# Kernel optimization log

Hardware: AMD Instinct MI355X
Metric: run time of the kernel (lower is better)

## Reference

```python
import jax, jax.numpy as jnp
import numpy as np

NX, N_IN, N_H1, N_H2, N_O = 65536, 2, 1024, 512, 1


def _deriv_tanh(h):
    # DerivTanh: 4 / (exp(-h^T) + exp(h^T))^2 == sech^2(h)^T, shape [features, nx]
    return 4.0 / (jnp.exp(-h.T) + jnp.exp(h.T)) ** 2


def setup_inputs() -> dict:
    key = jax.random.key(0)
    ks = jax.random.split(key, 7)

    def lin_init(k, fan_in, shape):
        bound = 1.0 / np.sqrt(fan_in)
        return jax.random.uniform(k, shape, jnp.float32, -bound, bound)

    x = jax.random.normal(ks[0], (NX, N_IN), jnp.float32)
    W1 = lin_init(ks[1], N_IN, (N_H1, N_IN))
    b1 = lin_init(ks[2], N_IN, (N_H1,))
    W2 = lin_init(ks[3], N_H1, (N_H2, N_H1))
    b2 = lin_init(ks[4], N_H1, (N_H2,))
    W3 = lin_init(ks[5], N_H2, (N_O, N_H2))
    b3 = lin_init(ks[6], N_H2, (N_O,))
    return {"x": x, "W1": W1, "b1": b1, "W2": W2, "b2": b2, "W3": W3, "b3": b3}


def reference(x, W1, b1, W2, b2, W3, b3):
    # Forward MLP
    h1 = x @ W1.T + b1          # [nx, h1]
    z1 = jnp.tanh(h1)
    h2 = z1 @ W2.T + b2         # [nx, h2]
    z2 = jnp.tanh(h2)
    y = z2 @ W3.T + b3          # [nx, 1]

    # Manual forward-mode derivative chain (transposed layout [features, nx])
    dz1dh1 = _deriv_tanh(h1)    # [h1, nx]
    dz2dh2 = _deriv_tanh(h2)    # [h2, nx]
    dh1dx1 = W1[:, 0][:, None]  # [h1, 1], broadcasts over nx (repeat in original)
    dh1dx2 = W1[:, 1][:, None]  # [h1, 1]

    dydx1 = (W3 @ (dz2dh2 * (W2 @ (dz1dh1 * dh1dx1)))).T  # [nx, 1]
    dydx2 = (W3 @ (dz2dh2 * (W2 @ (dz1dh1 * dh1dx2)))).T  # [nx, 1]

    v1 = dydx2
    v2 = -dydx1
    return (y, v1, v2)
```

## Files before the change

kernel.cpp:

```cpp
#include <hip/hip_runtime.h>


#define NXS    65536
#define SB     32
#define NBLK   2048
#define KSTEPS 8

typedef __attribute__((ext_vector_type(8)))  short bh8_t;
typedef __attribute__((ext_vector_type(4)))  unsigned int u32x4;
typedef __attribute__((ext_vector_type(16))) float fx16_t;
typedef unsigned int u32;

static __device__ __forceinline__ unsigned short f2bf(float f) {
  u32 u = __builtin_bit_cast(u32, f);
  u += 0x7FFFu + ((u >> 16) & 1u);
  return (unsigned short)(u >> 16);
}

static __device__ __forceinline__ u32 pkbf(float lo, float hi) {
  u32 r;
  asm("v_cvt_pk_bf16_f32 %0, %1, %2" : "=v"(r) : "v"(lo), "v"(hi));
  return r;
}

static __device__ __forceinline__ float fast_tanh(float h) {
  float e = __expf(2.0f * h);
  return 1.0f - 2.0f / (e + 1.0f);
}

__global__ void prep_all(const float* __restrict__ W2, const float* __restrict__ W1,
                         const float* __restrict__ b1, bh8_t* __restrict__ W2pT,
                         float4* __restrict__ W1b) {
  int f = blockIdx.x * 256 + threadIdx.x;
  int col = f & 31;
  int q   = (f >> 5) & 1;
  int nbk = (f >> 6) & 15;
  int kb  = f >> 10;
  const float* row = W2 + (nbk * 32 + col) * 1024 + kb * 16 + 4 * q;
  float4 lo = *(const float4*)(row);
  float4 hi = *(const float4*)(row + 8);
  bh8_t o;
  o[0] = (short)f2bf(lo.x); o[1] = (short)f2bf(lo.y);
  o[2] = (short)f2bf(lo.z); o[3] = (short)f2bf(lo.w);
  o[4] = (short)f2bf(hi.x); o[5] = (short)f2bf(hi.y);
  o[6] = (short)f2bf(hi.z); o[7] = (short)f2bf(hi.w);
  W2pT[f] = o;
  if (f < 1024) {
    float2 w = *(const float2*)(W1 + 2 * f);
    W1b[f] = make_float4(w.x, w.y, b1[f], 0.0f);
  }
}

__global__ __launch_bounds__(256, 2) void fused_kernel(
    const float* __restrict__ x,  const float4* __restrict__ W1b,
    const float* __restrict__ b2, const float* __restrict__ W3,
    const float* __restrict__ b3, const bh8_t* __restrict__ Bg,
    float* __restrict__ out)
{
  __shared__ __attribute__((aligned(16))) char smem[49152 + 1536];
  const int tid  = threadIdx.x;
  const int lane = tid & 63;
  const int wave = tid >> 6;
  const int q    = lane >> 5;
  const int col  = lane & 31;
  const int s0   = blockIdx.x * SB;

  const int gs  = tid & 31;
  const int gkb = tid >> 5;
  const float2 xv = *(const float2*)(x + 2 * (s0 + gs));
  const float x0 = xv.x, x1 = xv.y;
  const int wbase = (gs * 256) | (((gkb << 1) ^ (gs & 7)) << 4);

  fx16_t acc[3][4];
#pragma unroll
  for (int b = 0; b < 3; ++b)
#pragma unroll
    for (int nb = 0; nb < 4; ++nb)
#pragma unroll
      for (int r = 0; r < 16; ++r) acc[b][nb][r] = 0.0f;

  auto stageA = [&](int kt, char* Ab) {
    const int k16 = kt * 128 + gkb * 16;
#pragma unroll
    for (int gqp = 0; gqp < 2; ++gqp) {
      const int kL = k16 + 4 * gqp;
      u32x4 wz, wa0, wa1;
#pragma unroll
      for (int jp = 0; jp < 2; ++jp) {
        float4 cA = W1b[kL + 2 * jp];
        float4 cB = W1b[kL + 2 * jp + 1];
        float4 cC = W1b[kL + 8 + 2 * jp];
        float4 cD = W1b[kL + 8 + 2 * jp + 1];
        float hA = fmaf(x0, cA.x, fmaf(x1, cA.y, cA.z));
        float hB = fmaf(x0, cB.x, fmaf(x1, cB.y, cB.z));
        float hC = fmaf(x0, cC.x, fmaf(x1, cC.y, cC.z));
        float hD = fmaf(x0, cD.x, fmaf(x1, cD.y, cD.z));
        float zA = fast_tanh(hA), zB = fast_tanh(hB);
        float zC = fast_tanh(hC), zD = fast_tanh(hD);
        float dA = 1.f - zA * zA, dB = 1.f - zB * zB;
        float dC = 1.f - zC * zC, dD = 1.f - zD * zD;
        wz[jp]      = pkbf(zA, zB);
        wz[2 + jp]  = pkbf(zC, zD);
        wa0[jp]     = pkbf(dA * cA.x, dB * cB.x);
        wa0[2 + jp] = pkbf(dC * cC.x, dD * cD.x);
        wa1[jp]     = pkbf(dA * cA.y, dB * cB.y);
        wa1[2 + jp] = pkbf(dC * cC.y, dD * cD.y);
      }
      char* dst = Ab + (wbase ^ (gqp << 4));
      *(u32x4*)(dst)         = wz;
      *(u32x4*)(dst + 8192)  = wa0;
      *(u32x4*)(dst + 16384) = wa1;
    }
  };

  stageA(0, smem);
  __syncthreads();

  for (int kt = 0; kt < KSTEPS; ++kt) {
    char* Acur = smem + (kt & 1) * 24576;
    char* Anxt = smem + ((kt + 1) & 1) * 24576;
    if (kt + 1 < KSTEPS) stageA(kt + 1, Anxt);
    const int abase = col * 256;
#pragma unroll
    for (int ks = 0; ks < 8; ++ks) {
      const int uoff = (((2 * ks + q) ^ (col & 7)) << 4);
      bh8_t a0 = *(const bh8_t*)(Acur + abase + uoff);
      bh8_t a1 = *(const bh8_t*)(Acur + abase + 8192 + uoff);
      bh8_t a2 = *(const bh8_t*)(Acur + abase + 16384 + uoff);
      const int fb = ((kt * 8 + ks) * 16 + wave * 4) * 64 + lane;
      bh8_t bf0 = Bg[fb];
      bh8_t bf1 = Bg[fb + 64];
      bh8_t bf2 = Bg[fb + 128];
      bh8_t bf3 = Bg[fb + 192];
      __builtin_amdgcn_s_setprio(1);
      acc[0][0] = __builtin_amdgcn_mfma_f32_32x32x16_bf16(a0, bf0, acc[0][0], 0, 0, 0);
      acc[1][0] = __builtin_amdgcn_mfma_f32_32x32x16_bf16(a1, bf0, acc[1][0], 0, 0, 0);
      acc[2][0] = __builtin_amdgcn_mfma_f32_32x32x16_bf16(a2, bf0, acc[2][0], 0, 0, 0);
      acc[0][1] = __builtin_amdgcn_mfma_f32_32x32x16_bf16(a0, bf1, acc[0][1], 0, 0, 0);
      acc[1][1] = __builtin_amdgcn_mfma_f32_32x32x16_bf16(a1, bf1, acc[1][1], 0, 0, 0);
      acc[2][1] = __builtin_amdgcn_mfma_f32_32x32x16_bf16(a2, bf1, acc[2][1], 0, 0, 0);
      acc[0][2] = __builtin_amdgcn_mfma_f32_32x32x16_bf16(a0, bf2, acc[0][2], 0, 0, 0);
      acc[1][2] = __builtin_amdgcn_mfma_f32_32x32x16_bf16(a1, bf2, acc[1][2], 0, 0, 0);
      acc[2][2] = __builtin_amdgcn_mfma_f32_32x32x16_bf16(a2, bf2, acc[2][2], 0, 0, 0);
      acc[0][3] = __builtin_amdgcn_mfma_f32_32x32x16_bf16(a0, bf3, acc[0][3], 0, 0, 0);
      acc[1][3] = __builtin_amdgcn_mfma_f32_32x32x16_bf16(a1, bf3, acc[1][3], 0, 0, 0);
      acc[2][3] = __builtin_amdgcn_mfma_f32_32x32x16_bf16(a2, bf3, acc[2][3], 0, 0, 0);
      __builtin_amdgcn_s_setprio(0);
    }
    __syncthreads();
  }

  float b2n[4], w3n[4];
#pragma unroll
  for (int nb = 0; nb < 4; ++nb) {
    int n = wave * 128 + nb * 32 + col;
    b2n[nb] = b2[n];
    w3n[nb] = W3[n];
  }
  float* P = (float*)(smem + 49152);
#pragma unroll
  for (int r = 0; r < 16; ++r) {
    const int srow_o = (r & 3) + 8 * (r >> 2) + 4 * q;
    float py = 0.f, p1 = 0.f, p2 = 0.f;
#pragma unroll
    for (int nb = 0; nb < 4; ++nb) {
      float z2 = fast_tanh(acc[0][nb][r] + b2n[nb]);
      float d2 = 1.f - z2 * z2;
      py = fmaf(w3n[nb], z2, py);
      p1 = fmaf(w3n[nb] * d2, acc[1][nb][r], p1);
      p2 = fmaf(w3n[nb] * d2, acc[2][nb][r], p2);
    }
#pragma unroll
    for (int m = 1; m < 32; m <<= 1) {
      py += __shfl_xor(py, m, 64);
      p1 += __shfl_xor(p1, m, 64);
      p2 += __shfl_xor(p2, m, 64);
    }
    if (col == 0) {
      P[0 * 128 + srow_o * 4 + wave] = py;
      P[1 * 128 + srow_o * 4 + wave] = p1;
      P[2 * 128 + srow_o * 4 + wave] = p2;
    }
  }
  __syncthreads();
  if (tid < 96) {
    const int v = tid >> 5, s = tid & 31;
    const float* Pv = P + v * 128 + s * 4;
    float sum = Pv[0] + Pv[1] + Pv[2] + Pv[3];
    const int si = s0 + s;
    if (v == 0)      out[si]           = sum + b3[0];
    else if (v == 2) out[NXS + si]     = sum;
    else             out[2 * NXS + si] = -sum;
  }
}

extern "C" void kernel_launch(void* const* d_in, const int* in_sizes, int n_in,
                              void* d_out, int out_size, void* d_ws, size_t ws_size,
                              hipStream_t stream) {
  const float* x  = (const float*)d_in[0];
  const float* W1 = (const float*)d_in[1];
  const float* b1 = (const float*)d_in[2];
  const float* W2 = (const float*)d_in[3];
  const float* b2 = (const float*)d_in[4];
  const float* W3 = (const float*)d_in[5];
  const float* b3 = (const float*)d_in[6];
  bh8_t*  W2pT = (bh8_t*)d_ws;
  float4* W1b  = (float4*)((char*)d_ws + (1 << 20));

  prep_all<<<256, 256, 0, stream>>>(W2, W1, b1, W2pT, W1b);
  fused_kernel<<<NBLK, 256, 0, stream>>>(
      x, W1b, b2, W3, b3, (const bh8_t*)W2pT, (float*)d_out);
}
```

Before: 297.5 us.

## Software-pipeline A/B fragment loads and interleave layer-1 staging with MFMAs

Restructures the main loop so the next k-slice's A fragments (LDS) and B fragments (global) are prefetched into double-buffered registers while the current slice's 12 MFMAs issue. The layer-1 tanh/derivative staging for the next K tile is split into eight pair-sized chunks, one per inner step, so VALU/transcendental work overlaps the MFMA stream instead of running as a block before it. This is meant to hide load latency and make better use of the matrix pipeline, at the cost of more live registers (two A and B buffers plus staging vectors) and a possible occupancy or spill risk under launch_bounds(256,2).

```diff
diff --git a/kernel.cpp b/kernel.cpp
--- a/kernel.cpp
+++ b/kernel.cpp
@@ -6,9 +6,9 @@
 #define NBLK   2048
 #define KSTEPS 8
 
-typedef __attribute__((ext_vector_type(8)))  short bh8_t;
-typedef __attribute__((ext_vector_type(4)))  unsigned int u32x4;
-typedef __attribute__((ext_vector_type(16))) float fx16_t;
+typedef short bh8_t __attribute__((ext_vector_type(8)));
+typedef unsigned int u32x4 __attribute__((ext_vector_type(4)));
+typedef float fx16_t __attribute__((ext_vector_type(16)));
 typedef unsigned int u32;
 
 static __device__ __forceinline__ unsigned short f2bf(float f) {
@@ -71,85 +71,6 @@
   const float x0 = xv.x, x1 = xv.y;
   const int wbase = (gs * 256) | (((gkb << 1) ^ (gs & 7)) << 4);
 
-  fx16_t acc[3][4];
-#pragma unroll
-  for (int b = 0; b < 3; ++b)
-#pragma unroll
-    for (int nb = 0; nb < 4; ++nb)
-#pragma unroll
-      for (int r = 0; r < 16; ++r) acc[b][nb][r] = 0.0f;
-
-  auto stageA = [&](int kt, char* Ab) {
-    const int k16 = kt * 128 + gkb * 16;
-#pragma unroll
-    for (int gqp = 0; gqp < 2; ++gqp) {
-      const int kL = k16 + 4 * gqp;
-      u32x4 wz, wa0, wa1;
-#pragma unroll
-      for (int jp = 0; jp < 2; ++jp) {
-        float4 cA = W1b[kL + 2 * jp];
-        float4 cB = W1b[kL + 2 * jp + 1];
-        float4 cC = W1b[kL + 8 + 2 * jp];
-        float4 cD = W1b[kL + 8 + 2 * jp + 1];
-        float hA = fmaf(x0, cA.x, fmaf(x1, cA.y, cA.z));
-        float hB = fmaf(x0, cB.x, fmaf(x1, cB.y, cB.z));
-        float hC = fmaf(x0, cC.x, fmaf(x1, cC.y, cC.z));
-        float hD = fmaf(x0, cD.x, fmaf(x1, cD.y, cD.z));
-        float zA = fast_tanh(hA), zB = fast_tanh(hB);
-        float zC = fast_tanh(hC), zD = fast_tanh(hD);
-        float dA = 1.f - zA * zA, dB = 1.f - zB * zB;
-        float dC = 1.f - zC * zC, dD = 1.f - zD * zD;
-        wz[jp]      = pkbf(zA, zB);
-        wz[2 + jp]  = pkbf(zC, zD);
-        wa0[jp]     = pkbf(dA * cA.x, dB * cB.x);
-        wa0[2 + jp] = pkbf(dC * cC.x, dD * cD.x);
-        wa1[jp]     = pkbf(dA * cA.y, dB * cB.y);
-        wa1[2 + jp] = pkbf(dC * cC.y, dD * cD.y);
-      }
-      char* dst = Ab + (wbase ^ (gqp << 4));
-      *(u32x4*)(dst)         = wz;
-      *(u32x4*)(dst + 8192)  = wa0;
-      *(u32x4*)(dst + 16384) = wa1;
-    }
-  };
-
-  stageA(0, smem);
-  __syncthreads();
-
-  for (int kt = 0; kt < KSTEPS; ++kt) {
-    char* Acur = smem + (kt & 1) * 24576;
-    char* Anxt = smem + ((kt + 1) & 1) * 24576;
-    if (kt + 1 < KSTEPS) stageA(kt + 1, Anxt);
-    const int abase = col * 256;
-#pragma unroll
-    for (int ks = 0; ks < 8; ++ks) {
-      const int uoff = (((2 * ks + q) ^ (col & 7)) << 4);
-      bh8_t a0 = *(const bh8_t*)(Acur + abase + uoff);
-      bh8_t a1 = *(const bh8_t*)(Acur + abase + 8192 + uoff);
-      bh8_t a2 = *(const bh8_t*)(Acur + abase + 16384 + uoff);
-      const int fb = ((kt * 8 + ks) * 16 + wave * 4) * 64 + lane;
-      bh8_t bf0 = Bg[fb];
-      bh8_t bf1 = Bg[fb + 64];
-      bh8_t bf2 = Bg[fb + 128];
-      bh8_t bf3 = Bg[fb + 192];
-      __builtin_amdgcn_s_setprio(1);
-      acc[0][0] = __builtin_amdgcn_mfma_f32_32x32x16_bf16(a0, bf0, acc[0][0], 0, 0, 0);
-      acc[1][0] = __builtin_amdgcn_mfma_f32_32x32x16_bf16(a1, bf0, acc[1][0], 0, 0, 0);
-      acc[2][0] = __builtin_amdgcn_mfma_f32_32x32x16_bf16(a2, bf0, acc[2][0], 0, 0, 0);
-      acc[0][1] = __builtin_amdgcn_mfma_f32_32x32x16_bf16(a0, bf1, acc[0][1], 0, 0, 0);
-      acc[1][1] = __builtin_amdgcn_mfma_f32_32x32x16_bf16(a1, bf1, acc[1][1], 0, 0, 0);
-      acc[2][1] = __builtin_amdgcn_mfma_f32_32x32x16_bf16(a2, bf1, acc[2][1], 0, 0, 0);
-      acc[0][2] = __builtin_amdgcn_mfma_f32_32x32x16_bf16(a0, bf2, acc[0][2], 0, 0, 0);
-      acc[1][2] = __builtin_amdgcn_mfma_f32_32x32x16_bf16(a1, bf2, acc[1][2], 0, 0, 0);
-      acc[2][2] = __builtin_amdgcn_mfma_f32_32x32x16_bf16(a2, bf2, acc[2][2], 0, 0, 0);
-      acc[0][3] = __builtin_amdgcn_mfma_f32_32x32x16_bf16(a0, bf3, acc[0][3], 0, 0, 0);
-      acc[1][3] = __builtin_amdgcn_mfma_f32_32x32x16_bf16(a1, bf3, acc[1][3], 0, 0, 0);
-      acc[2][3] = __builtin_amdgcn_mfma_f32_32x32x16_bf16(a2, bf3, acc[2][3], 0, 0, 0);
-      __builtin_amdgcn_s_setprio(0);
-    }
-    __syncthreads();
-  }
-
   float b2n[4], w3n[4];
 #pragma unroll
   for (int nb = 0; nb < 4; ++nb) {
@@ -157,6 +78,89 @@
     b2n[nb] = b2[n];
     w3n[nb] = W3[n];
   }
+
+  fx16_t acc[3][4];
+#pragma unroll
+  for (int b = 0; b < 3; ++b)
+#pragma unroll
+    for (int nb = 0; nb < 4; ++nb)
+#pragma unroll
+      for (int r = 0; r < 16; ++r) acc[b][nb][r] = 0.0f;
+
+  bh8_t Ar[2][3], Br[2][4];
+  u32x4 sz, sv0, sv1;
+
+  auto loadB = [&](int kt, int ks, bh8_t* B) {
+    const int fb = ((kt * 8 + ks) * 16 + wave * 4) * 64 + lane;
+    B[0] = Bg[fb];
+    B[1] = Bg[fb + 64];
+    B[2] = Bg[fb + 128];
+    B[3] = Bg[fb + 192];
+  };
+  auto loadA = [&](const char* Ab, int ks, bh8_t* A) {
+    const int uoff = (((2 * ks + q) ^ (col & 7)) << 4);
+    const char* p = Ab + col * 256 + uoff;
+    A[0] = *(const bh8_t*)(p);
+    A[1] = *(const bh8_t*)(p + 8192);
+    A[2] = *(const bh8_t*)(p + 16384);
+  };
+  auto stage_pair = [&](int ktA, char* Ab, int p) {
+    const int gqp = p >> 2, jp = (p >> 1) & 1, half = p & 1;
+    const int k0 = ktA * 128 + gkb * 16 + gqp * 4 + half * 8 + 2 * jp;
+    float4 cA = W1b[k0];
+    float4 cB = W1b[k0 + 1];
+    float hA = fmaf(x0, cA.x, fmaf(x1, cA.y, cA.z));
+    float hB = fmaf(x0, cB.x, fmaf(x1, cB.y, cB.z));
+    float zA = fast_tanh(hA), zB = fast_tanh(hB);
+    float dA = 1.f - zA * zA, dB = 1.f - zB * zB;
+    const int slot = half * 2 + jp;
+    sz[slot]  = pkbf(zA, zB);
+    sv0[slot] = pkbf(dA * cA.x, dB * cB.x);
+    sv1[slot] = pkbf(dA * cA.y, dB * cB.y);
+    if ((p & 3) == 3) {
+      char* dst = Ab + (wbase ^ (gqp << 4));
+      *(u32x4*)(dst)         = sz;
+      *(u32x4*)(dst + 8192)  = sv0;
+      *(u32x4*)(dst + 16384) = sv1;
+    }
+  };
+  auto mfma12 = [&](const bh8_t* A, const bh8_t* B) {
+    __builtin_amdgcn_s_setprio(1);
+#pragma unroll
+    for (int nb = 0; nb < 4; ++nb) {
+      acc[0][nb] = __builtin_amdgcn_mfma_f32_32x32x16_bf16(A[0], B[nb], acc[0][nb], 0, 0, 0);
+      acc[1][nb] = __builtin_amdgcn_mfma_f32_32x32x16_bf16(A[1], B[nb], acc[1][nb], 0, 0, 0);
+      acc[2][nb] = __builtin_amdgcn_mfma_f32_32x32x16_bf16(A[2], B[nb], acc[2][nb], 0, 0, 0);
+    }
+    __builtin_amdgcn_s_setprio(0);
+  };
+
+  loadB(0, 0, Br[0]);
+#pragma unroll
+  for (int p = 0; p < 8; ++p) stage_pair(0, smem, p);
+  __syncthreads();
+  loadA(smem, 0, Ar[0]);
+
+  for (int kt = 0; kt < KSTEPS; ++kt) {
+    char* Acur = smem + (kt & 1) * 24576;
+    char* Anxt = smem + ((kt + 1) & 1) * 24576;
+    const bool more = (kt + 1 < KSTEPS);
+#pragma unroll
+    for (int ks = 0; ks < 8; ++ks) {
+      const int cb = ks & 1, nbuf = cb ^ 1;
+      if (ks < 7) {
+        loadB(kt, ks + 1, Br[nbuf]);
+        loadA(Acur, ks + 1, Ar[nbuf]);
+      } else if (more) {
+        loadB(kt + 1, 0, Br[nbuf]);
+      }
+      if (more) stage_pair(kt + 1, Anxt, ks);
+      mfma12(Ar[cb], Br[cb]);
+    }
+    __syncthreads();
+    if (more) loadA(Anxt, 0, Ar[0]);
+  }
+
   float* P = (float*)(smem + 49152);
 #pragma unroll
   for (int r = 0; r < 16; ++r) {
```

Result: slower. 888.7 us (+198.8%).
